# Optimization experiments

Hardware: AMD Instinct MI355X
Metric: run time of the kernel (lower is better)

## Reference

```python
import jax, jax.numpy as jnp
import numpy as np

B, T, C, H = 2, 2048, 1024, 16
D = C // H


def setup_inputs() -> dict:
    key = jax.random.key(0)
    k1, k2, k3 = jax.random.split(key, 3)
    x = jax.random.normal(k1, (B, T, C), dtype=jnp.float32)
    w_attn = jax.random.normal(k2, (3 * C, C), dtype=jnp.float32) * (1.0 / np.sqrt(C))
    w_proj = jax.random.normal(k3, (C, C), dtype=jnp.float32) * (1.0 / np.sqrt(C))
    # causal mask, 1 = keep, 0 = masked (matches att.masked_fill(mask == 0, -inf))
    mask = jnp.tril(jnp.ones((T, T), dtype=jnp.int32))[None, None, :, :]
    return {"x": x, "w_attn": w_attn, "w_proj": w_proj, "mask": mask}


def reference(x, w_attn, w_proj, mask):
    Bq, Tq, Cq = x.shape
    qkv = x @ w_attn.T                      # [B,T,3C] (torch Linear: x @ W^T)
    q, k, v = jnp.split(qkv, 3, axis=2)
    # [B,T,C] -> [B,H,T,D]
    q = q.reshape(Bq, Tq, H, D).transpose(0, 2, 1, 3)
    k = k.reshape(Bq, Tq, H, D).transpose(0, 2, 1, 3)
    v = v.reshape(Bq, Tq, H, D).transpose(0, 2, 1, 3)
    att = jnp.einsum("bhqd,bhkd->bhqk", q, k) * (1.0 / np.sqrt(D))
    att = jnp.where(mask == 0, -jnp.inf, att)
    att = jax.nn.softmax(att, axis=-1)      # dropout p=0.0 -> identity
    y = jnp.einsum("bhqk,bhkd->bhqd", att, v)
    y = y.transpose(0, 2, 1, 3).reshape(Bq, Tq, Cq)
    return y @ w_proj.T
```

## Files before the change

kernel.cpp:

```cpp
#include <hip/hip_runtime.h>
#include <hip/hip_bf16.h>
#include <math.h>


typedef __attribute__((ext_vector_type(4))) float floatx4;
typedef __attribute__((ext_vector_type(8))) __bf16 bf16x8;

#define MFMA_BF16(a, b, c) __builtin_amdgcn_mfma_f32_16x16x32_bf16((a), (b), (c), 0, 0, 0)

typedef __attribute__((address_space(1))) const uint32_t* gas_t;
typedef __attribute__((address_space(3))) uint32_t* las_t;
__device__ inline void gl2lds16(const void* g, void* l) {
    __builtin_amdgcn_global_load_lds((gas_t)g, (las_t)l, 16, 0, 0);
}

__device__ inline uint4 cvt8_f32_bf16(const float4 a, const float4 b) {
    union { __hip_bfloat16 h[8]; uint4 u; } c;
    c.h[0] = __float2bfloat16(a.x); c.h[1] = __float2bfloat16(a.y);
    c.h[2] = __float2bfloat16(a.z); c.h[3] = __float2bfloat16(a.w);
    c.h[4] = __float2bfloat16(b.x); c.h[5] = __float2bfloat16(b.y);
    c.h[6] = __float2bfloat16(b.z); c.h[7] = __float2bfloat16(b.w);
    return c.u;
}

__global__ __launch_bounds__(256) void cvt_all(
    const float* __restrict__ x, const float* __restrict__ wa,
    const float* __restrict__ wp, __hip_bfloat16* __restrict__ out)
{
    const size_t e = ((size_t)blockIdx.x * 256 + threadIdx.x) * 8;
    const float* src; size_t off;
    if (e < 4194304)      { src = x;  off = e; }
    else if (e < 7340032) { src = wa; off = e - 4194304; }
    else                  { src = wp; off = e - 7340032; }
    const float4 a = *(const float4*)&src[off];
    const float4 b = *(const float4*)&src[off + 4];
    *(uint4*)&out[e] = cvt8_f32_bf16(a, b);
}

__global__ __launch_bounds__(256) void gemm_qkv(
    const __hip_bfloat16* __restrict__ A,
    const __hip_bfloat16* __restrict__ Bt,
    __hip_bfloat16* __restrict__ qk,
    __hip_bfloat16* __restrict__ vt, int K)
{
    __shared__ __hip_bfloat16 As0[128][32];
    __shared__ __hip_bfloat16 As1[128][32];
    __shared__ __hip_bfloat16 Bs0[128][32];
    __shared__ __hip_bfloat16 Bs1[128][32];

    const int tid  = threadIdx.x;
    const int wave = tid >> 6;
    const int lane = tid & 63;
    const int quad = lane >> 4;
    const int l15  = lane & 15;
    const int wrow = wave >> 1;
    const int wcol = wave & 1;
    const int bm = blockIdx.y * 128;
    const int bn = blockIdx.x * 128;

    floatx4 acc[4][4];
#pragma unroll
    for (int i = 0; i < 4; ++i)
#pragma unroll
        for (int j = 0; j < 4; ++j)
            acc[i][j] = (floatx4){0.f, 0.f, 0.f, 0.f};

    const int srow = lane >> 2;
    const int scol = (lane & 3) * 8;

    const __hip_bfloat16* Abase = A  + (size_t)bm * K;
    const __hip_bfloat16* Bbase = Bt + (size_t)bn * K;

    for (int k0 = 0; k0 < K; k0 += 64) {
#pragma unroll
        for (int c = 0; c < 2; ++c) {
            const int rbase = wave * 32 + c * 16;
            const size_t ga = (size_t)(rbase + srow) * K + k0 + scol;
            gl2lds16(&Abase[ga],      &As0[rbase][0]);
            gl2lds16(&Abase[ga + 32], &As1[rbase][0]);
            gl2lds16(&Bbase[ga],      &Bs0[rbase][0]);
            gl2lds16(&Bbase[ga + 32], &Bs1[rbase][0]);
        }
        __syncthreads();

#pragma unroll
        for (int kd = 0; kd < 2; ++kd) {
            const __hip_bfloat16 (*Ap)[32] = kd ? As1 : As0;
            const __hip_bfloat16 (*Bp)[32] = kd ? Bs1 : Bs0;
            bf16x8 af[4], bfv[4];
#pragma unroll
            for (int i = 0; i < 4; ++i)
                af[i] = *(const bf16x8*)&Ap[wrow * 64 + i * 16 + l15][quad * 8];
#pragma unroll
            for (int j = 0; j < 4; ++j)
                bfv[j] = *(const bf16x8*)&Bp[wcol * 64 + j * 16 + l15][quad * 8];
#pragma unroll
            for (int i = 0; i < 4; ++i)
#pragma unroll
                for (int j = 0; j < 4; ++j)
                    acc[i][j] = MFMA_BF16(af[i], bfv[j], acc[i][j]);
        }
        __syncthreads();
    }

    if (bn < 2048) {
        const float sc = (bn < 1024) ? 0.18033688f : 1.0f;
#pragma unroll
        for (int i = 0; i < 4; ++i)
#pragma unroll
            for (int j = 0; j < 4; ++j)
#pragma unroll
                for (int r = 0; r < 4; ++r) {
                    const int row = bm + wrow * 64 + i * 16 + quad * 4 + r;
                    const int col = bn + wcol * 64 + j * 16 + l15;
                    qk[(size_t)row * 2048 + col] = __float2bfloat16(acc[i][j][r] * sc);
                }
    } else {
#pragma unroll
        for (int i = 0; i < 4; ++i)
#pragma unroll
            for (int j = 0; j < 4; ++j) {
                const int trow0 = bm + wrow * 64 + i * 16 + quad * 4;
                const int d = bn - 2048 + wcol * 64 + j * 16 + l15;
                const int b = trow0 >> 11, t0 = trow0 & 2047;
                union { __hip_bfloat16 h[4]; uint2 u; } pk;
#pragma unroll
                for (int r = 0; r < 4; ++r) pk.h[r] = __float2bfloat16(acc[i][j][r]);
                *(uint2*)&vt[((size_t)(b * 16 + (d >> 6)) * 64 + (d & 63)) * 2048 + t0] = pk.u;
            }
    }
}

__global__ __launch_bounds__(256) void gemm_bt_mfma_n64(
    const __hip_bfloat16* __restrict__ A,
    const __hip_bfloat16* __restrict__ Bt,
    float* __restrict__ C, int M, int N, int K)
{
    __shared__ __hip_bfloat16 As[128][32];
    __shared__ __hip_bfloat16 Bs[64][32];

    const int tid  = threadIdx.x;
    const int wave = tid >> 6;
    const int lane = tid & 63;
    const int quad = lane >> 4;
    const int l15  = lane & 15;
    const int wrow = wave >> 1;
    const int wcol = wave & 1;
    const int bm = blockIdx.y * 128;
    const int bn = blockIdx.x * 64;

    floatx4 acc[4][2];
#pragma unroll
    for (int i = 0; i < 4; ++i)
#pragma unroll
        for (int j = 0; j < 2; ++j)
            acc[i][j] = (floatx4){0.f, 0.f, 0.f, 0.f};

    const int srow = lane >> 2;
    const int scol = (lane & 3) * 8;

    const __hip_bfloat16* Abase = A  + (size_t)bm * K;
    const __hip_bfloat16* Bbase = Bt + (size_t)bn * K;

    for (int k0 = 0; k0 < K; k0 += 32) {
        {
            const int ra0 = wave * 32;
            gl2lds16(&Abase[(size_t)(ra0 + srow) * K + k0 + scol], &As[ra0][0]);
            gl2lds16(&Abase[(size_t)(ra0 + 16 + srow) * K + k0 + scol], &As[ra0 + 16][0]);
            const int rb0 = wave * 16;
            gl2lds16(&Bbase[(size_t)(rb0 + srow) * K + k0 + scol], &Bs[rb0][0]);
        }
        __syncthreads();

        bf16x8 af[4], bfv[2];
#pragma unroll
        for (int i = 0; i < 4; ++i)
            af[i] = *(const bf16x8*)&As[wrow * 64 + i * 16 + l15][quad * 8];
#pragma unroll
        for (int j = 0; j < 2; ++j)
            bfv[j] = *(const bf16x8*)&Bs[wcol * 32 + j * 16 + l15][quad * 8];

#pragma unroll
        for (int i = 0; i < 4; ++i)
#pragma unroll
            for (int j = 0; j < 2; ++j)
                acc[i][j] = MFMA_BF16(af[i], bfv[j], acc[i][j]);
        __syncthreads();
    }

#pragma unroll
    for (int i = 0; i < 4; ++i)
#pragma unroll
        for (int j = 0; j < 2; ++j)
#pragma unroll
            for (int r = 0; r < 4; ++r) {
                const int row = bm + wrow * 64 + i * 16 + quad * 4 + r;
                const int col = bn + wcol * 32 + j * 16 + l15;
                C[(size_t)row * N + col] = acc[i][j][r];
            }
}

__global__ __launch_bounds__(256) void attn_kernel(
    const __hip_bfloat16* __restrict__ qk,
    const __hip_bfloat16* __restrict__ vt,
    float* __restrict__ part)
{
    constexpr int T = 2048;
    __shared__ __hip_bfloat16 Ks[64][72];
    __shared__ __hip_bfloat16 Vt[64][72];
    __shared__ __hip_bfloat16 PsA[64][72];
    __shared__ __hip_bfloat16 PsB[64][72];

    const int bh = blockIdx.x;
    const int b = bh >> 4, h = bh & 15;
    const int p = blockIdx.y;
    const int s = blockIdx.z;
    const int q0A = p * 64;
    const int q0B = (31 - p) * 64;

    const int tid  = threadIdx.x;
    const int wave = tid >> 6;
    const int lane = tid & 63;
    const int quad = lane >> 4;
    const int l15  = lane & 15;

    const __hip_bfloat16* base  = qk + (size_t)b * T * 2048;
    const __hip_bfloat16* vbase = vt + (size_t)((b * 16 + h) * 64) * 2048;

    bf16x8 aqA[2], aqB[2];
#pragma unroll
    for (int kd = 0; kd < 2; ++kd) {
        aqA[kd] = *(const bf16x8*)&base[(size_t)(q0A + wave * 16 + l15) * 2048 + h * 64 + kd * 32 + quad * 8];
        aqB[kd] = *(const bf16x8*)&base[(size_t)(q0B + wave * 16 + l15) * 2048 + h * 64 + kd * 32 + quad * 8];
    }

    bf16x8 ones;
#pragma unroll
    for (int i = 0; i < 8; ++i) ones[i] = (__bf16)1.0f;

    floatx4 accA[4], accB[4], lA, lB;
#pragma unroll
    for (int r = 0; r < 4; ++r) {
        accA[r] = (floatx4){0.f, 0.f, 0.f, 0.f};
        accB[r] = (floatx4){0.f, 0.f, 0.f, 0.f};
    }
    lA = (floatx4){0.f, 0.f, 0.f, 0.f};
    lB = (floatx4){0.f, 0.f, 0.f, 0.f};

    const int sr = tid >> 2;
    const int sc = (tid & 3) * 16;

    for (int j0 = s * 64; j0 <= q0B; j0 += 128) {
        const bool actA = (j0 <= q0A);
        const bool dgA  = (j0 == q0A);
        const bool dgB  = (j0 == q0B);

        {
            const size_t kg = (size_t)(j0 + sr) * 2048 + 1024 + h * 64 + sc;
            *(uint4*)&Ks[sr][sc]     = *(const uint4*)&base[kg];
            *(uint4*)&Ks[sr][sc + 8] = *(const uint4*)&base[kg + 8];
            const size_t vg = (size_t)sr * 2048 + j0 + sc;
            *(uint4*)&Vt[sr][sc]     = *(const uint4*)&vbase[vg];
            *(uint4*)&Vt[sr][sc + 8] = *(const uint4*)&vbase[vg + 8];
        }
        __syncthreads();

        floatx4 sA[4], sB[4];
#pragma unroll
        for (int jt = 0; jt < 4; ++jt) {
            sA[jt] = (floatx4){0.f, 0.f, 0.f, 0.f};
            sB[jt] = (floatx4){0.f, 0.f, 0.f, 0.f};
        }
#pragma unroll
        for (int jt = 0; jt < 4; ++jt)
#pragma unroll
            for (int kd = 0; kd < 2; ++kd) {
                bf16x8 bk = *(const bf16x8*)&Ks[jt * 16 + l15][kd * 32 + quad * 8];
                sB[jt] = MFMA_BF16(aqB[kd], bk, sB[jt]);
                if (actA) sA[jt] = MFMA_BF16(aqA[kd], bk, sA[jt]);
            }

        const int myrow = wave * 16 + quad * 4;
#pragma unroll
        for (int jt = 0; jt < 4; ++jt) {
            const int col = jt * 16 + l15;
#pragma unroll
            for (int r = 0; r < 4; ++r) {
                float pv = __builtin_amdgcn_exp2f(sB[jt][r]);
                if (dgB && col > (myrow + r)) pv = 0.f;
                PsB[myrow + r][col] = __float2bfloat16(pv);
            }
            if (actA) {
#pragma unroll
                for (int r = 0; r < 4; ++r) {
                    float pv = __builtin_amdgcn_exp2f(sA[jt][r]);
                    if (dgA && col > (myrow + r)) pv = 0.f;
                    PsA[myrow + r][col] = __float2bfloat16(pv);
                }
            }
        }
        __syncthreads();

#pragma unroll
        for (int kk = 0; kk < 2; ++kk) {
            bf16x8 apB = *(const bf16x8*)&PsB[wave * 16 + l15][kk * 32 + quad * 8];
            bf16x8 apA;
            if (actA) apA = *(const bf16x8*)&PsA[wave * 16 + l15][kk * 32 + quad * 8];
            lB = MFMA_BF16(apB, ones, lB);
            if (actA) lA = MFMA_BF16(apA, ones, lA);
#pragma unroll
            for (int jd = 0; jd < 4; ++jd) {
                bf16x8 bv = *(const bf16x8*)&Vt[jd * 16 + l15][kk * 32 + quad * 8];
                accB[jd] = MFMA_BF16(apB, bv, accB[jd]);
                if (actA) accA[jd] = MFMA_BF16(apA, bv, accA[jd]);
            }
        }
        __syncthreads();
    }

    float* pA = part + (size_t)((s * 32 + bh) * 32 + p) * 4160;
    float* pB = part + (size_t)((s * 32 + bh) * 32 + (31 - p)) * 4160;
#pragma unroll
    for (int jd = 0; jd < 4; ++jd)
#pragma unroll
        for (int r = 0; r < 4; ++r) {
            const int row = wave * 16 + quad * 4 + r;
            const int col = jd * 16 + l15;
            pA[row * 64 + col] = accA[jd][r];
            pB[row * 64 + col] = accB[jd][r];
        }
    if (l15 == 0) {
#pragma unroll
        for (int r = 0; r < 4; ++r) {
            const int row = wave * 16 + quad * 4 + r;
            pA[4096 + row] = lA[r];
            pB[4096 + row] = lB[r];
        }
    }
}

__global__ __launch_bounds__(256) void combine_kernel(
    const float* __restrict__ part, __hip_bfloat16* __restrict__ y)
{
    const int bh = blockIdx.x, t = blockIdx.y;
    const int b = bh >> 4, h = bh & 15;
    const float* p0 = part + (size_t)((0 * 32 + bh) * 32 + t) * 4160;
    const float* p1 = part + (size_t)((1 * 32 + bh) * 32 + t) * 4160;

    __shared__ float linv[64];
    const int tid = threadIdx.x;
    if (tid < 64) linv[tid] = 1.f / (p0[4096 + tid] + p1[4096 + tid]);
    __syncthreads();

    const int row = tid >> 2;
    const int c0  = (tid & 3) * 16;
    const float inv = linv[row];

    union { __hip_bfloat16 h[16]; uint4 u[2]; } ob;
#pragma unroll
    for (int c = 0; c < 4; ++c) {
        const float4 a = *(const float4*)&p0[row * 64 + c0 + c * 4];
        const float4 d = *(const float4*)&p1[row * 64 + c0 + c * 4];
        ob.h[c * 4 + 0] = __float2bfloat16((a.x + d.x) * inv);
        ob.h[c * 4 + 1] = __float2bfloat16((a.y + d.y) * inv);
        ob.h[c * 4 + 2] = __float2bfloat16((a.z + d.z) * inv);
        ob.h[c * 4 + 3] = __float2bfloat16((a.w + d.w) * inv);
    }
    __hip_bfloat16* yp = &y[((size_t)(b * 2048 + t * 64 + row)) * 1024 + h * 64 + c0];
    *(uint4*)(yp)     = ob.u[0];
    *(uint4*)(yp + 8) = ob.u[1];
}

extern "C" void kernel_launch(void* const* d_in, const int* in_sizes, int n_in,
                              void* d_out, int out_size, void* d_ws, size_t ws_size,
                              hipStream_t stream)
{
    const float* x      = (const float*)d_in[0];
    const float* w_attn = (const float*)d_in[1];
    const float* w_proj = (const float*)d_in[2];

    float* out = (float*)d_out;
    __hip_bfloat16* xb  = (__hip_bfloat16*)d_ws;
    __hip_bfloat16* wab = xb  + (size_t)4096 * 1024;
    __hip_bfloat16* wpb = wab + (size_t)3072 * 1024;
    __hip_bfloat16* qkb = wpb + (size_t)1024 * 1024;
    __hip_bfloat16* y   = qkb + (size_t)4096 * 2048;
    __hip_bfloat16* vt  = y   + (size_t)4096 * 1024;
    float*          prt = (float*)(vt + (size_t)2048 * 2048);

    cvt_all<<<4096, 256, 0, stream>>>(x, w_attn, w_proj, xb);

    gemm_qkv<<<dim3(24, 32), 256, 0, stream>>>(xb, wab, qkb, vt, 1024);

    attn_kernel<<<dim3(32, 16, 2), 256, 0, stream>>>(qkb, vt, prt);
    combine_kernel<<<dim3(32, 32), 256, 0, stream>>>(prt, y);

    gemm_bt_mfma_n64<<<dim3(16, 32), 256, 0, stream>>>(y, wpb, out, 4096, 1024, 1024);
}
```

Baseline: 209.7 us.

## Keep attention probabilities in registers via transposed S^T MFMA formulation

Computes S^T = K·Q^T so each lane's MFMA accumulator already sits in B-operand layout for the P·V product. P is then passed straight from registers as zero-padded bf16x8 fragments, which removes the PsA/PsB shared-memory round trip and one __syncthreads per tile. The output partials are written transposed, and the combine kernel transposes them back through an LDS tile. The cost is that half of each P·V MFMA's K dimension is zero padding, so the P·V and row-sum steps issue twice as many MFMAs.

```diff
diff --git a/kernel.cpp b/kernel.cpp
--- a/kernel.cpp
+++ b/kernel.cpp
@@ -5,6 +5,7 @@
 
 typedef __attribute__((ext_vector_type(4))) float floatx4;
 typedef __attribute__((ext_vector_type(8))) __bf16 bf16x8;
+typedef __attribute__((ext_vector_type(4))) __bf16 bf16x4;
 
 #define MFMA_BF16(a, b, c) __builtin_amdgcn_mfma_f32_16x16x32_bf16((a), (b), (c), 0, 0, 0)
 
@@ -208,8 +209,6 @@
     constexpr int T = 2048;
     __shared__ __hip_bfloat16 Ks[64][72];
     __shared__ __hip_bfloat16 Vt[64][72];
-    __shared__ __hip_bfloat16 PsA[64][72];
-    __shared__ __hip_bfloat16 PsB[64][72];
 
     const int bh = blockIdx.x;
     const int b = bh >> 4, h = bh & 15;
@@ -237,18 +236,20 @@
     bf16x8 ones;
 #pragma unroll
     for (int i = 0; i < 8; ++i) ones[i] = (__bf16)1.0f;
-
-    floatx4 accA[4], accB[4], lA, lB;
+    const bf16x4 zero4 = {};
+
+    floatx4 accA[4], accB[4], lTA, lTB;
 #pragma unroll
     for (int r = 0; r < 4; ++r) {
         accA[r] = (floatx4){0.f, 0.f, 0.f, 0.f};
         accB[r] = (floatx4){0.f, 0.f, 0.f, 0.f};
     }
-    lA = (floatx4){0.f, 0.f, 0.f, 0.f};
-    lB = (floatx4){0.f, 0.f, 0.f, 0.f};
+    lTA = (floatx4){0.f, 0.f, 0.f, 0.f};
+    lTB = (floatx4){0.f, 0.f, 0.f, 0.f};
 
     const int sr = tid >> 2;
     const int sc = (tid & 3) * 16;
+    const int myq = wave * 16 + l15;
 
     for (int j0 = s * 64; j0 <= q0B; j0 += 128) {
         const bool actA = (j0 <= q0A);
@@ -275,46 +276,49 @@
         for (int jt = 0; jt < 4; ++jt)
 #pragma unroll
             for (int kd = 0; kd < 2; ++kd) {
-                bf16x8 bk = *(const bf16x8*)&Ks[jt * 16 + l15][kd * 32 + quad * 8];
-                sB[jt] = MFMA_BF16(aqB[kd], bk, sB[jt]);
-                if (actA) sA[jt] = MFMA_BF16(aqA[kd], bk, sA[jt]);
-            }
-
-        const int myrow = wave * 16 + quad * 4;
+                bf16x8 ak = *(const bf16x8*)&Ks[jt * 16 + l15][kd * 32 + quad * 8];
+                sB[jt] = MFMA_BF16(ak, aqB[kd], sB[jt]);
+                if (actA) sA[jt] = MFMA_BF16(ak, aqA[kd], sA[jt]);
+            }
+
+        bf16x8 pfA[4], pfB[4];
 #pragma unroll
         for (int jt = 0; jt < 4; ++jt) {
-            const int col = jt * 16 + l15;
+            const int kvl = jt * 16 + quad * 4;
+            bf16x4 lo;
 #pragma unroll
             for (int r = 0; r < 4; ++r) {
                 float pv = __builtin_amdgcn_exp2f(sB[jt][r]);
-                if (dgB && col > (myrow + r)) pv = 0.f;
-                PsB[myrow + r][col] = __float2bfloat16(pv);
-            }
+                if (dgB && (kvl + r) > myq) pv = 0.f;
+                lo[r] = (__bf16)__float2bfloat16(pv);
+            }
+            pfB[jt] = __builtin_shufflevector(lo, zero4, 0, 1, 2, 3, 4, 5, 6, 7);
             if (actA) {
 #pragma unroll
                 for (int r = 0; r < 4; ++r) {
                     float pv = __builtin_amdgcn_exp2f(sA[jt][r]);
-                    if (dgA && col > (myrow + r)) pv = 0.f;
-                    PsA[myrow + r][col] = __float2bfloat16(pv);
+                    if (dgA && (kvl + r) > myq) pv = 0.f;
+                    lo[r] = (__bf16)__float2bfloat16(pv);
                 }
-            }
-        }
-        __syncthreads();
-
-#pragma unroll
-        for (int kk = 0; kk < 2; ++kk) {
-            bf16x8 apB = *(const bf16x8*)&PsB[wave * 16 + l15][kk * 32 + quad * 8];
-            bf16x8 apA;
-            if (actA) apA = *(const bf16x8*)&PsA[wave * 16 + l15][kk * 32 + quad * 8];
-            lB = MFMA_BF16(apB, ones, lB);
-            if (actA) lA = MFMA_BF16(apA, ones, lA);
-#pragma unroll
-            for (int jd = 0; jd < 4; ++jd) {
-                bf16x8 bv = *(const bf16x8*)&Vt[jd * 16 + l15][kk * 32 + quad * 8];
-                accB[jd] = MFMA_BF16(apB, bv, accB[jd]);
-                if (actA) accA[jd] = MFMA_BF16(apA, bv, accA[jd]);
-            }
-        }
+                pfA[jt] = __builtin_shufflevector(lo, zero4, 0, 1, 2, 3, 4, 5, 6, 7);
+            }
+        }
+
+#pragma unroll
+        for (int jt = 0; jt < 4; ++jt) {
+            lTB = MFMA_BF16(ones, pfB[jt], lTB);
+            if (actA) lTA = MFMA_BF16(ones, pfA[jt], lTA);
+        }
+
+#pragma unroll
+        for (int jd = 0; jd < 4; ++jd)
+#pragma unroll
+            for (int jt = 0; jt < 4; ++jt) {
+                const bf16x4 vlo = *(const bf16x4*)&Vt[jd * 16 + l15][jt * 16 + quad * 4];
+                const bf16x8 av = __builtin_shufflevector(vlo, zero4, 0, 1, 2, 3, 4, 5, 6, 7);
+                accB[jd] = MFMA_BF16(av, pfB[jt], accB[jd]);
+                if (actA) accA[jd] = MFMA_BF16(av, pfA[jt], accA[jd]);
+            }
         __syncthreads();
     }
 
@@ -324,18 +328,13 @@
     for (int jd = 0; jd < 4; ++jd)
 #pragma unroll
         for (int r = 0; r < 4; ++r) {
-            const int row = wave * 16 + quad * 4 + r;
-            const int col = jd * 16 + l15;
-            pA[row * 64 + col] = accA[jd][r];
-            pB[row * 64 + col] = accB[jd][r];
-        }
-    if (l15 == 0) {
-#pragma unroll
-        for (int r = 0; r < 4; ++r) {
-            const int row = wave * 16 + quad * 4 + r;
-            pA[4096 + row] = lA[r];
-            pB[4096 + row] = lB[r];
-        }
+            const int d = jd * 16 + quad * 4 + r;
+            pA[d * 64 + myq] = accA[jd][r];
+            pB[d * 64 + myq] = accB[jd][r];
+        }
+    if (quad == 0) {
+        pA[4096 + myq] = lTA[0];
+        pB[4096 + myq] = lTB[0];
     }
 }
 
@@ -347,26 +346,32 @@
     const float* p0 = part + (size_t)((0 * 32 + bh) * 32 + t) * 4160;
     const float* p1 = part + (size_t)((1 * 32 + bh) * 32 + t) * 4160;
 
+    __shared__ float Ls[64][65];
     __shared__ float linv[64];
     const int tid = threadIdx.x;
     if (tid < 64) linv[tid] = 1.f / (p0[4096 + tid] + p1[4096 + tid]);
+
+    const int dr = tid >> 2;
+    const int q0 = (tid & 3) * 16;
+#pragma unroll
+    for (int c = 0; c < 4; ++c) {
+        const float4 a = *(const float4*)&p0[dr * 64 + q0 + c * 4];
+        const float4 e = *(const float4*)&p1[dr * 64 + q0 + c * 4];
+        Ls[dr][q0 + c * 4 + 0] = a.x + e.x;
+        Ls[dr][q0 + c * 4 + 1] = a.y + e.y;
+        Ls[dr][q0 + c * 4 + 2] = a.z + e.z;
+        Ls[dr][q0 + c * 4 + 3] = a.w + e.w;
+    }
     __syncthreads();
 
-    const int row = tid >> 2;
-    const int c0  = (tid & 3) * 16;
-    const float inv = linv[row];
-
-    union { __hip_bfloat16 h[16]; uint4 u[2]; } ob;
-#pragma unroll
-    for (int c = 0; c < 4; ++c) {
-        const float4 a = *(const float4*)&p0[row * 64 + c0 + c * 4];
-        const float4 d = *(const float4*)&p1[row * 64 + c0 + c * 4];
-        ob.h[c * 4 + 0] = __float2bfloat16((a.x + d.x) * inv);
-        ob.h[c * 4 + 1] = __float2bfloat16((a.y + d.y) * inv);
-        ob.h[c * 4 + 2] = __float2bfloat16((a.z + d.z) * inv);
-        ob.h[c * 4 + 3] = __float2bfloat16((a.w + d.w) * inv);
-    }
-    __hip_bfloat16* yp = &y[((size_t)(b * 2048 + t * 64 + row)) * 1024 + h * 64 + c0];
+    const int q  = tid >> 2;
+    const int d0 = (tid & 3) * 16;
+    const float inv = linv[q];
+    union { __hip_bfloat16 hh[16]; uint4 u[2]; } ob;
+#pragma unroll
+    for (int j = 0; j < 16; ++j)
+        ob.hh[j] = __float2bfloat16(Ls[d0 + j][q] * inv);
+    __hip_bfloat16* yp = &y[((size_t)(b * 2048 + t * 64 + q)) * 1024 + h * 64 + d0];
     *(uint4*)(yp)     = ob.u[0];
     *(uint4*)(yp + 8) = ob.u[1];
 }
```

After: 212.7 us. No clear change (+1.4%).
